# Kernel tuning notes

Measured on AMD Instinct MI355X. Metric: run time of the kernel, lower is better.

## Reference

```python
import jax, jax.numpy as jnp
import numpy as np

B, N_NODES, VOCAB, H = 128, 1023, 2048, 256  # depth-9 perfect binary trees (heap layout)


def setup_inputs() -> dict:
    key = jax.random.key(0)
    k1, k2, k3, k4, k5 = jax.random.split(key, 5)
    tokens = jax.random.randint(k1, (B, N_NODES), 0, VOCAB)
    emb = jax.random.normal(k2, (VOCAB, H), dtype=jnp.float32) * 0.02
    Wx = jax.random.normal(k3, (H, 5 * H), dtype=jnp.float32) * 0.02
    Ul = jax.random.normal(k4, (H, 5 * H), dtype=jnp.float32) * 0.02
    Ur = jax.random.normal(k5, (H, 5 * H), dtype=jnp.float32) * 0.02
    b = jnp.zeros((5 * H,), dtype=jnp.float32)
    return {"tokens": tokens, "emb": emb, "Wx": Wx, "Ul": Ul, "Ur": Ur, "b": b}


def _tree_lstm(tokens, emb, Wx, Ul, Ur, b):
    # tokens: [B, 2^(D+1)-1] in level-order heap layout; children of heap index i
    # are 2i+1, 2i+2 -> within level d+1 they sit at offsets 2k, 2k+1.
    n_nodes = tokens.shape[1]
    depth = int(np.log2(n_nodes + 1)) - 1
    hdim = emb.shape[1]
    x_all = emb[tokens]  # [B, N, H] embedding lookup (memory-bound gather)
    h = c = None
    for d in range(depth, -1, -1):  # bottom-up over levels (fixed structural loop)
        start, n = 2 ** d - 1, 2 ** d
        x = x_all[:, start:start + n]  # [B, n, H]
        gates = jnp.einsum('bnh,hg->bng', x, Wx) + b
        if h is not None:
            hl, hr = h[:, 0::2], h[:, 1::2]
            cl, cr = c[:, 0::2], c[:, 1::2]
            gates = gates + jnp.einsum('bnh,hg->bng', hl, Ul) + jnp.einsum('bnh,hg->bng', hr, Ur)
        i, fl, fr, o, u = jnp.split(gates, 5, axis=-1)
        i, fl, fr, o = map(jax.nn.sigmoid, (i, fl, fr, o))
        u = jnp.tanh(u)
        c_new = i * u
        if c is not None:
            c_new = c_new + fl * cl + fr * cr
        c = c_new
        h = o * jnp.tanh(c)
    return h[:, 0], c[:, 0]  # root states, each [B, H]


def reference(tokens, emb, Wx, Ul, Ur, b):
    h_root, _ = _tree_lstm(tokens, emb, Wx, Ul, Ur, b)
    return h_root  # [B, H]
```

## Files before the change

kernel.cpp:

```cpp
#include <hip/hip_runtime.h>
#include <hip/hip_bf16.h>
#include <math.h>

#define B_SZ   128
#define HDIM   256
#define NG     1280
#define NNODES 1023
#define VOCAB  2048

typedef unsigned int uint32;
typedef short  short8v  __attribute__((ext_vector_type(8)));
typedef float  float4v  __attribute__((ext_vector_type(4)));

__device__ __forceinline__ float sigm(float x) {
    return 1.0f / (1.0f + __expf(-x));
}
__device__ __forceinline__ float tanh_fast(float x) {
    return 2.0f / (1.0f + __expf(-2.0f * x)) - 1.0f;
}
__device__ __forceinline__ float bf2f(unsigned short u) {
    return __uint_as_float(((uint32)u) << 16);
}
__device__ __forceinline__ unsigned short f2bf(float f) {
    uint32 x = __float_as_uint(f);
    uint32 r = (x + 0x7FFFu + ((x >> 16) & 1u)) >> 16;
    return (unsigned short)r;
}

__device__ __forceinline__ void dma16(const unsigned short* gptr, unsigned short* lptr) {
    __builtin_amdgcn_global_load_lds(
        (const __attribute__((address_space(1))) void*)gptr,
        (__attribute__((address_space(3))) void*)lptr, 16, 0, 0);
}

__global__ __launch_bounds__(256) void embb_kernel(
    const float* __restrict__ emb, unsigned short* __restrict__ embb)
{
    const int t = blockIdx.x * 256 + threadIdx.x;
    const float4 v0 = *(const float4*)(emb + (size_t)t * 8);
    const float4 v1 = *(const float4*)(emb + (size_t)t * 8 + 4);
    short8v o;
    o[0] = (short)f2bf(v0.x); o[1] = (short)f2bf(v0.y);
    o[2] = (short)f2bf(v0.z); o[3] = (short)f2bf(v0.w);
    o[4] = (short)f2bf(v1.x); o[5] = (short)f2bf(v1.y);
    o[6] = (short)f2bf(v1.z); o[7] = (short)f2bf(v1.w);
    *(short8v*)(embb + (size_t)t * 8) = o;
}

__global__ __launch_bounds__(256) void prep_wtf(
    const float* __restrict__ Ul, const float* __restrict__ Ur,
    const float* __restrict__ Wx, unsigned short* __restrict__ WTf)
{
    const int t = blockIdx.x * 256 + threadIdx.x;
    const int l = t & 63;
    const int q = l >> 4, c = l & 15;
    const int ks = (t >> 6) % 24;
    const int ng = t / (24 * 64);
    const int col = ng * 16 + c;
    const int k = ks * 32 + q * 8;
    const float* src = (k < 256) ? (Ul + (size_t)k * NG + col)
                     : (k < 512) ? (Ur + (size_t)(k - 256) * NG + col)
                                 : (Wx + (size_t)(k - 512) * NG + col);
    short8v v;
    #pragma unroll
    for (int j = 0; j < 8; ++j) v[j] = (short)f2bf(src[(size_t)j * NG]);
    *(short8v*)(WTf + (size_t)t * 8) = v;
}

__global__ __launch_bounds__(256, 2) void ewb_mfma(
    const unsigned short* __restrict__ WTf, const unsigned short* __restrict__ embb,
    const float* __restrict__ bias, unsigned short* __restrict__ EWb)
{
    __shared__ __align__(16) unsigned short Ab[2][4096];
    __shared__ __align__(16) unsigned short wbE[20480];

    const int tid  = threadIdx.x;
    const int lane = tid & 63;
    const int w    = tid >> 6;
    const int quad = lane >> 4, col15 = lane & 15;
    const int jt = blockIdx.x;
    const int rowBase = blockIdx.y * 64;
    const int jbase   = jt * 64;

    const unsigned short* agp[2];
    unsigned short* ldst[2];
    #pragma unroll
    for (int t = 0; t < 2; ++t) {
        const int ch = 2 * w + t, sub = ch >> 2, rt = ch & 3;
        const int srow = rowBase + rt * 16 + col15;
        agp[t]  = embb + (size_t)srow * HDIM + sub * 32 + quad * 8;
        ldst[t] = &Ab[0][0] + ch * 512;
    }

    const short8v* WTfv = (const short8v*)WTf;
    uint32 boff[5];
    #pragma unroll
    for (int g = 0; g < 5; ++g)
        boff[g] = ((g * 16 + jt * 4 + w) * 24 + 16) * 64 + lane;

    float4v acc[4][5];
    #pragma unroll
    for (int rt = 0; rt < 4; ++rt)
        #pragma unroll
        for (int g = 0; g < 5; ++g)
            #pragma unroll
            for (int e = 0; e < 4; ++e) acc[rt][g][e] = 0.0f;

    dma16(agp[0], ldst[0]); dma16(agp[1], ldst[1]);
    __syncthreads();

    #pragma unroll
    for (int s = 0; s < 4; ++s) {
        if (s < 3) {
            dma16(agp[0] + (s + 1) * 64, ldst[0] + ((s + 1) & 1) * 4096);
            dma16(agp[1] + (s + 1) * 64, ldst[1] + ((s + 1) & 1) * 4096);
        }
        #pragma unroll
        for (int sub = 0; sub < 2; ++sub) {
            short8v bf[5];
            #pragma unroll
            for (int g = 0; g < 5; ++g) bf[g] = WTfv[boff[g] + (s * 2 + sub) * 64];
            #pragma unroll
            for (int rt = 0; rt < 4; ++rt) {
                const short8v af = *(const short8v*)&Ab[s & 1][(sub * 4 + rt) * 512 + lane * 8];
                #pragma unroll
                for (int g = 0; g < 5; ++g)
                    acc[rt][g] = __builtin_amdgcn_mfma_f32_16x16x32_bf16(
                        af, bf[g], acc[rt][g], 0, 0, 0);
            }
        }
        __syncthreads();
    }

    const int jl = w * 16 + col15;
    const int j  = jbase + jl;
    float bz[5];
    #pragma unroll
    for (int g = 0; g < 5; ++g) bz[g] = bias[g * 256 + j];
    const int jchunk = jl >> 3, jpos = jl & 7;

    #pragma unroll
    for (int rt = 0; rt < 4; ++rt) {
        #pragma unroll
        for (int reg = 0; reg < 4; ++reg) {
            const int rr = rt * 16 + quad * 4 + reg;
            const int roff = ((jchunk + 2 * quad) & 7) * 8 + jpos;
            #pragma unroll
            for (int g = 0; g < 5; ++g)
                wbE[(g * 64 + rr) * 64 + roff] = f2bf(acc[rt][g][reg] + bz[g]);
        }
    }
    __syncthreads();

    #pragma unroll
    for (int k2 = 0; k2 < 10; ++k2) {
        const int c = tid + k2 * 256;
        const int g = c >> 9, rr = (c >> 3) & 63, u = c & 7;
        const int ru = (u + 2 * ((rr >> 2) & 3)) & 7;
        const short8v v = *(const short8v*)&wbE[(g * 64 + rr) * 64 + ru * 8];
        *(short8v*)(EWb + (size_t)(rowBase + rr) * NG + g * 256 + jbase + u * 8) = v;
    }
}

__global__ __launch_bounds__(256) void leaftab_kernel(
    const unsigned short* __restrict__ EWb,
    unsigned short* __restrict__ Hleaf, unsigned short* __restrict__ Cleaf)
{
    const int t = blockIdx.x * 256 + threadIdx.x;
    const int tok = t >> 8, j = t & 255;
    const float gi = bf2f(EWb[(size_t)tok * NG + j]);
    const float go = bf2f(EWb[(size_t)tok * NG + 768 + j]);
    const float gu = bf2f(EWb[(size_t)tok * NG + 1024 + j]);
    const float c = sigm(gi) * tanh_fast(gu);
    const float h = sigm(go) * tanh_fast(c);
    Hleaf[t] = f2bf(h);
    Cleaf[t] = f2bf(c);
}

__global__ __launch_bounds__(256, 2) void level_kernel(
    const unsigned short* __restrict__ WTf, const unsigned short* __restrict__ EWb,
    const int* __restrict__ tokens,
    const unsigned short* __restrict__ Hleaf, const unsigned short* __restrict__ Cleaf,
    const unsigned short* __restrict__ hsrc, const unsigned short* __restrict__ csrc,
    unsigned short* __restrict__ hdst, unsigned short* __restrict__ cdst,
    float* __restrict__ out, const int d)
{
    const int n = 1 << d;

    __shared__ __align__(16) unsigned short Ab[2][4096];

    const int tid  = threadIdx.x;
    const int lane = tid & 63;
    const int w    = tid >> 6;
    const int quad = lane >> 4, col15 = lane & 15;
    const int jt = blockIdx.x;
    const int rowBase = blockIdx.y * 64;
    const int jbase   = jt * 64;

    const unsigned short* agp_lo[2];
    const unsigned short* agp_hi[2];
    unsigned short* ldst[2];
    #pragma unroll
    for (int t = 0; t < 2; ++t) {
        const int ch = 2 * w + t, sub = ch >> 2, rt = ch & 3;
        const int srow = rowBase + rt * 16 + col15;
        if (d == 8) {
            const int b = srow >> 8, i = srow & 255;
            const int tokL = tokens[b * NNODES + 511 + 2 * i];
            const int tokR = tokens[b * NNODES + 512 + 2 * i];
            agp_lo[t] = Hleaf + (size_t)tokL * HDIM + sub * 32 + quad * 8;
            agp_hi[t] = Hleaf + (size_t)tokR * HDIM + sub * 32 + quad * 8;
        } else {
            agp_lo[t] = hsrc + (size_t)(2 * srow) * HDIM + sub * 32 + quad * 8;
            agp_hi[t] = agp_lo[t] + HDIM;
        }
        ldst[t] = &Ab[0][0] + ch * 512;
    }

    const short8v* WTfv = (const short8v*)WTf;
    uint32 boff[5];
    #pragma unroll
    for (int g = 0; g < 5; ++g)
        boff[g] = ((g * 16 + jt * 4 + w) * 24) * 64 + lane;

    float4v acc[4][5];
    #pragma unroll
    for (int rt = 0; rt < 4; ++rt)
        #pragma unroll
        for (int g = 0; g < 5; ++g)
            #pragma unroll
            for (int e = 0; e < 4; ++e) acc[rt][g][e] = 0.0f;

    dma16(agp_lo[0], ldst[0]); dma16(agp_lo[1], ldst[1]);
    __syncthreads();

    #pragma unroll
    for (int s = 0; s < 8; ++s) {
        if (s < 7) {
            const int sn = s + 1;
            #pragma unroll
            for (int t = 0; t < 2; ++t) {
                const unsigned short* p = (sn < 4) ? (agp_lo[t] + sn * 64)
                                                   : (agp_hi[t] + (sn - 4) * 64);
                dma16(p, ldst[t] + (sn & 1) * 4096);
            }
        }

        #pragma unroll
        for (int sub = 0; sub < 2; ++sub) {
            short8v bf[5];
            #pragma unroll
            for (int g = 0; g < 5; ++g) bf[g] = WTfv[boff[g] + (s * 2 + sub) * 64];
            #pragma unroll
            for (int rt = 0; rt < 4; ++rt) {
                const short8v af = *(const short8v*)&Ab[s & 1][(sub * 4 + rt) * 512 + lane * 8];
                #pragma unroll
                for (int g = 0; g < 5; ++g)
                    acc[rt][g] = __builtin_amdgcn_mfma_f32_16x16x32_bf16(
                        af, bf[g], acc[rt][g], 0, 0, 0);
            }
        }
        __syncthreads();
    }

    const int jl = w * 16 + col15;
    const int j  = jbase + jl;
    float hv[4][4], cv[4][4];
    #pragma unroll
    for (int rt = 0; rt < 4; ++rt) {
        #pragma unroll
        for (int reg = 0; reg < 4; ++reg) {
            const int rr = rt * 16 + quad * 4 + reg;
            const int grow = rowBase + rr;
            const int tok = tokens[(grow >> d) * NNODES + (n - 1) + (grow & (n - 1))];
            const unsigned short* ewp = EWb + (size_t)tok * NG + j;
            float cl, cr;
            if (d == 8) {
                const int b = grow >> 8, i = grow & 255;
                const int tokL = tokens[b * NNODES + 511 + 2 * i];
                const int tokR = tokens[b * NNODES + 512 + 2 * i];
                cl = bf2f(Cleaf[(size_t)tokL * HDIM + j]);
                cr = bf2f(Cleaf[(size_t)tokR * HDIM + j]);
            } else {
                cl = bf2f(csrc[(size_t)(2 * grow) * HDIM + j]);
                cr = bf2f(csrc[(size_t)(2 * grow + 1) * HDIM + j]);
            }
            const float gi  = acc[rt][0][reg] + bf2f(ewp[0]);
            const float gfl = acc[rt][1][reg] + bf2f(ewp[256]);
            const float gfr = acc[rt][2][reg] + bf2f(ewp[512]);
            const float go  = acc[rt][3][reg] + bf2f(ewp[768]);
            const float gu  = acc[rt][4][reg] + bf2f(ewp[1024]);
            const float ii = sigm(gi), fl = sigm(gfl), fr = sigm(gfr), oo = sigm(go);
            const float uu = tanh_fast(gu);
            const float c = ii * uu + fl * cl + fr * cr;
            const float h = oo * tanh_fast(c);
            cv[rt][reg] = c; hv[rt][reg] = h;
            if (d == 0) out[(size_t)grow * HDIM + j] = h;
        }
    }
    if (d == 0) return;

    unsigned short* wb = &Ab[0][0];
    const int jchunk = jl >> 3, jpos = jl & 7;
    #pragma unroll
    for (int rt = 0; rt < 4; ++rt) {
        #pragma unroll
        for (int reg = 0; reg < 4; ++reg) {
            const int rr = rt * 16 + quad * 4 + reg;
            const int roff = ((jchunk + 2 * quad) & 7) * 8 + jpos;
            wb[rr * 64 + roff]        = f2bf(hv[rt][reg]);
            wb[4096 + rr * 64 + roff] = f2bf(cv[rt][reg]);
        }
    }
    __syncthreads();
    #pragma unroll
    for (int k2 = 0; k2 < 4; ++k2) {
        const int c = tid + k2 * 256;
        const int arr = c >> 9, rr = (c >> 3) & 63, u = c & 7;
        const int ru = (u + 2 * ((rr >> 2) & 3)) & 7;
        const short8v v = *(const short8v*)(wb + (arr * 4096 + rr * 64 + ru * 8));
        unsigned short* dstp = (arr ? cdst : hdst) +
            (size_t)(rowBase + rr) * HDIM + jbase + u * 8;
        *(short8v*)dstp = v;
    }
}

extern "C" void kernel_launch(void* const* d_in, const int* in_sizes, int n_in,
                              void* d_out, int out_size, void* d_ws, size_t ws_size,
                              hipStream_t stream)
{
    const int*   tokens = (const int*)d_in[0];
    const float* emb    = (const float*)d_in[1];
    const float* Wx     = (const float*)d_in[2];
    const float* Ul     = (const float*)d_in[3];
    const float* Ur     = (const float*)d_in[4];
    const float* bias   = (const float*)d_in[5];
    float* out = (float*)d_out;

    const size_t EW_ELEMS  = (size_t)VOCAB * NG;
    const size_t EMB_ELEMS = (size_t)VOCAB * HDIM;
    const size_t WTF_ELEMS = (size_t)80 * 24 * 64 * 8;
    const size_t LT_ELEMS  = (size_t)VOCAB * HDIM;
    const size_t SLOT_A    = (size_t)16384 * HDIM;
    const size_t SLOT_B    = (size_t)32768 * HDIM;
    const size_t REQUIRED  = (EW_ELEMS + EMB_ELEMS + WTF_ELEMS + 2 * LT_ELEMS
                              + 2 * (SLOT_A + SLOT_B)) * 2;
    if (ws_size < REQUIRED || d_ws == nullptr) return;

    char* ws = (char*)d_ws;
    unsigned short* EWb   = (unsigned short*)ws;
    unsigned short* embb  = EWb + EW_ELEMS;
    unsigned short* WTf   = embb + EMB_ELEMS;
    unsigned short* Hleaf = WTf + WTF_ELEMS;
    unsigned short* Cleaf = Hleaf + LT_ELEMS;
    unsigned short* hA    = Cleaf + LT_ELEMS;
    unsigned short* cA    = hA + SLOT_A;
    unsigned short* hB    = cA + SLOT_A;
    unsigned short* cB    = hB + SLOT_B;

    embb_kernel<<<dim3(256), 256, 0, stream>>>(emb, embb);
    prep_wtf<<<dim3(480), 256, 0, stream>>>(Ul, Ur, Wx, WTf);
    ewb_mfma<<<dim3(4, 32), 256, 0, stream>>>(WTf, embb, bias, EWb);
    leaftab_kernel<<<dim3(2048), 256, 0, stream>>>(EWb, Hleaf, Cleaf);

    for (int d = 8; d >= 0; --d) {
        const int NRB = 2 << d;
        const bool evenD = ((d & 1) == 0);
        const unsigned short* hs = evenD ? hA : hB;
        const unsigned short* cs = evenD ? cA : cB;
        unsigned short* hd = evenD ? hB : hA;
        unsigned short* cd = evenD ? cB : cA;
        level_kernel<<<dim3(4, NRB), 256, 0, stream>>>(
            WTf, EWb, tokens, Hleaf, Cleaf, hs, cs, hd, cd, out, d);
    }
}
```

Measured before the change: 367.2 us.

## Fuse Wx input projection into level GEMM instead of gathering precomputed EWb

Result: slower. 378.3 us (+3.0%).

```diff
diff --git a/kernel.cpp b/kernel.cpp
--- a/kernel.cpp
+++ b/kernel.cpp
@@ -178,10 +178,11 @@
 }
 
 __global__ __launch_bounds__(256, 2) void level_kernel(
-    const unsigned short* __restrict__ WTf, const unsigned short* __restrict__ EWb,
-    const int* __restrict__ tokens,
+    const unsigned short* __restrict__ WTf, const int* __restrict__ tokens,
+    const unsigned short* __restrict__ embb,
     const unsigned short* __restrict__ Hleaf, const unsigned short* __restrict__ Cleaf,
     const unsigned short* __restrict__ hsrc, const unsigned short* __restrict__ csrc,
+    const float* __restrict__ bias,
     unsigned short* __restrict__ hdst, unsigned short* __restrict__ cdst,
     float* __restrict__ out, const int d)
 {
@@ -199,13 +200,16 @@
 
     const unsigned short* agp_lo[2];
     const unsigned short* agp_hi[2];
+    const unsigned short* agp_x[2];
     unsigned short* ldst[2];
     #pragma unroll
     for (int t = 0; t < 2; ++t) {
         const int ch = 2 * w + t, sub = ch >> 2, rt = ch & 3;
         const int srow = rowBase + rt * 16 + col15;
+        const int b = srow >> d, i = srow & (n - 1);
+        const int tokN = tokens[b * NNODES + (n - 1) + i];
+        agp_x[t] = embb + (size_t)tokN * HDIM + sub * 32 + quad * 8;
         if (d == 8) {
-            const int b = srow >> 8, i = srow & 255;
             const int tokL = tokens[b * NNODES + 511 + 2 * i];
             const int tokR = tokens[b * NNODES + 512 + 2 * i];
             agp_lo[t] = Hleaf + (size_t)tokL * HDIM + sub * 32 + quad * 8;
@@ -223,6 +227,12 @@
     for (int g = 0; g < 5; ++g)
         boff[g] = ((g * 16 + jt * 4 + w) * 24) * 64 + lane;
 
+    const int jl = w * 16 + col15;
+    const int j  = jbase + jl;
+    float bz[5];
+    #pragma unroll
+    for (int g = 0; g < 5; ++g) bz[g] = bias[g * 256 + j];
+
     float4v acc[4][5];
     #pragma unroll
     for (int rt = 0; rt < 4; ++rt)
@@ -235,13 +245,14 @@
     __syncthreads();
 
     #pragma unroll
-    for (int s = 0; s < 8; ++s) {
-        if (s < 7) {
+    for (int s = 0; s < 12; ++s) {
+        if (s < 11) {
             const int sn = s + 1;
             #pragma unroll
             for (int t = 0; t < 2; ++t) {
                 const unsigned short* p = (sn < 4) ? (agp_lo[t] + sn * 64)
-                                                   : (agp_hi[t] + (sn - 4) * 64);
+                                        : (sn < 8) ? (agp_hi[t] + (sn - 4) * 64)
+                                                   : (agp_x[t]  + (sn - 8) * 64);
                 dma16(p, ldst[t] + (sn & 1) * 4096);
             }
         }
@@ -263,8 +274,6 @@
         __syncthreads();
     }
 
-    const int jl = w * 16 + col15;
-    const int j  = jbase + jl;
     float hv[4][4], cv[4][4];
     #pragma unroll
     for (int rt = 0; rt < 4; ++rt) {
@@ -272,8 +281,6 @@
         for (int reg = 0; reg < 4; ++reg) {
             const int rr = rt * 16 + quad * 4 + reg;
             const int grow = rowBase + rr;
-            const int tok = tokens[(grow >> d) * NNODES + (n - 1) + (grow & (n - 1))];
-            const unsigned short* ewp = EWb + (size_t)tok * NG + j;
             float cl, cr;
             if (d == 8) {
                 const int b = grow >> 8, i = grow & 255;
@@ -285,11 +292,11 @@
                 cl = bf2f(csrc[(size_t)(2 * grow) * HDIM + j]);
                 cr = bf2f(csrc[(size_t)(2 * grow + 1) * HDIM + j]);
             }
-            const float gi  = acc[rt][0][reg] + bf2f(ewp[0]);
-            const float gfl = acc[rt][1][reg] + bf2f(ewp[256]);
-            const float gfr = acc[rt][2][reg] + bf2f(ewp[512]);
-            const float go  = acc[rt][3][reg] + bf2f(ewp[768]);
-            const float gu  = acc[rt][4][reg] + bf2f(ewp[1024]);
+            const float gi  = acc[rt][0][reg] + bz[0];
+            const float gfl = acc[rt][1][reg] + bz[1];
+            const float gfr = acc[rt][2][reg] + bz[2];
+            const float go  = acc[rt][3][reg] + bz[3];
+            const float gu  = acc[rt][4][reg] + bz[4];
             const float ii = sigm(gi), fl = sigm(gfl), fr = sigm(gfr), oo = sigm(go);
             const float uu = tanh_fast(gu);
             const float c = ii * uu + fl * cl + fr * cr;
@@ -371,6 +378,6 @@
         unsigned short* hd = evenD ? hB : hA;
         unsigned short* cd = evenD ? cB : cA;
         level_kernel<<<dim3(4, NRB), 256, 0, stream>>>(
-            WTf, EWb, tokens, Hleaf, Cleaf, hs, cs, hd, cd, out, d);
-    }
-}
+            WTf, tokens, embb, Hleaf, Cleaf, hs, cs, bias, hd, cd, out, d);
+    }
+}
```
